# Kernel tuning notes

Hardware: AMD Instinct MI355X
Metric: run time of the kernel (lower is better)

Reference implementation:

```python
import jax, jax.numpy as jnp
import numpy as np

EMBED_DIM = 1024


def setup_inputs() -> dict:
    key = jax.random.key(0)
    ks = jax.random.split(key, 9)
    d = EMBED_DIM
    s = 1.0 / np.sqrt(d)
    x = jax.random.normal(ks[0], (4, 4096, d), dtype=jnp.float32)
    Wq = jax.random.normal(ks[1], (d, d), dtype=jnp.float32) * s
    bq = jax.random.normal(ks[2], (d,), dtype=jnp.float32) * 0.01
    Wk = jax.random.normal(ks[3], (d, d), dtype=jnp.float32) * s
    bk = jax.random.normal(ks[4], (d,), dtype=jnp.float32) * 0.01
    Wv = jax.random.normal(ks[5], (d, d), dtype=jnp.float32) * s
    bv = jax.random.normal(ks[6], (d,), dtype=jnp.float32) * 0.01
    Wo = jax.random.normal(ks[7], (d, d), dtype=jnp.float32) * s
    bo = jax.random.normal(ks[8], (d,), dtype=jnp.float32) * 0.01
    return {"x": x, "Wq": Wq, "bq": bq, "Wk": Wk, "bk": bk,
            "Wv": Wv, "bv": bv, "Wo": Wo, "bo": bo}


def reference(x, Wq, bq, Wk, bk, Wv, bv, Wo, bo):
    # x: [b, s, d]; single-head attention, scale = 1/sqrt(d)
    b, s, d = x.shape
    q = x @ Wq + bq
    k = x @ Wk + bk
    v = x @ Wv + bv
    scale = 1.0 / jnp.sqrt(jnp.asarray(d, x.dtype))
    scores = jnp.einsum('bqd,bkd->bqk', q, k) * scale  # [b, s, s]
    causal = jnp.tril(jnp.ones((s, s), dtype=bool))
    scores = jnp.where(causal, scores, jnp.asarray(-jnp.inf, scores.dtype))
    attn = jax.nn.softmax(scores, axis=-1)
    ctx = jnp.einsum('bqk,bkd->bqd', attn, v)
    return ctx @ Wo + bo
```

## Files before the change

### kernel.cpp

```cpp
#include <hip/hip_runtime.h>


typedef unsigned short u16;
typedef __attribute__((ext_vector_type(4))) unsigned short u16x4;
typedef __attribute__((ext_vector_type(8))) unsigned short u16x8;
typedef __attribute__((ext_vector_type(8))) __bf16 bf16x8;
typedef __attribute__((ext_vector_type(4))) float f32x4;

typedef const __attribute__((address_space(1))) void* as1cp;
typedef __attribute__((address_space(3))) void* as3p;

struct GemmPtrs {
  const u16* A[4];
  const u16* B[4];
  const float* bias[4];
  void* C[4];
};
struct TransPtrs {
  const void* in[4];
  u16* out[4];
};
struct SmPtrs {
  u16* P[4];
};

__device__ __forceinline__ u16 f2bf(float f) {
  union { float f; unsigned int i; } c; c.f = f;
  unsigned int r = c.i + 0x7fffu + ((c.i >> 16) & 1u);
  return (u16)(r >> 16);
}
__device__ __forceinline__ float bf2f(u16 u) {
  union { unsigned int i; float f; } c; c.i = ((unsigned int)u) << 16;
  return c.f;
}

__global__ __launch_bounds__(256) void cast_f32_bf16(const float* __restrict__ in,
                                                     u16* __restrict__ out, int n4) {
  int i = blockIdx.x * blockDim.x + threadIdx.x;
  if (i >= n4) return;
  float4 v = ((const float4*)in)[i];
  u16x4 u;
  u.x = f2bf(v.x); u.y = f2bf(v.y); u.z = f2bf(v.z); u.w = f2bf(v.w);
  ((u16x4*)out)[i] = u;
}

template <bool IN_F32>
__global__ __launch_bounds__(256) void transpose_to_bf16(TransPtrs tp, int R, int C) {
  __shared__ u16 t[32][34];
  int z = blockIdx.z;
  int tx = threadIdx.x, ty = threadIdx.y;
  int c0 = blockIdx.x * 32, r0 = blockIdx.y * 32;
#pragma unroll
  for (int dy = 0; dy < 4; ++dy) {
    int r = r0 + ty + dy * 8;
    int c = c0 + tx;
    u16 hv;
    if (IN_F32) hv = f2bf(((const float*)tp.in[z])[(size_t)r * C + c]);
    else        hv = ((const u16*)tp.in[z])[(size_t)r * C + c];
    t[ty + dy * 8][tx] = hv;
  }
  __syncthreads();
  u16* op = tp.out[z];
#pragma unroll
  for (int dy = 0; dy < 4; ++dy) {
    int a = ty + dy * 8;
    op[(size_t)(c0 + a) * R + r0 + tx] = t[tx][a];
  }
}

__global__ __launch_bounds__(256) void softmax_causal(SmPtrs sp) {
  int row = blockIdx.x;
  u16* P = sp.P[blockIdx.y];
  int tid = threadIdx.x;
  int lane = tid & 63, wv = tid >> 6;
  u16x8* prow = (u16x8*)(P + (size_t)row * 4096);
  int nch = (row >> 3) + 1;
  int fend = ((row >> 7) + 1) << 4;
  int c0 = tid, c1 = tid + 256;
  bool a0 = c0 < nch, a1 = c1 < nch;
  float vals[16];
  float lmax = -3.0e38f;
  if (a0) {
    u16x8 u = prow[c0];
#pragma unroll
    for (int e = 0; e < 8; ++e) {
      float f = (c0 * 8 + e <= row) ? bf2f(u[e]) : -3.0e38f;
      vals[e] = f; lmax = fmaxf(lmax, f);
    }
  } else {
#pragma unroll
    for (int e = 0; e < 8; ++e) vals[e] = -3.0e38f;
  }
  if (a1) {
    u16x8 u = prow[c1];
#pragma unroll
    for (int e = 0; e < 8; ++e) {
      float f = (c1 * 8 + e <= row) ? bf2f(u[e]) : -3.0e38f;
      vals[8 + e] = f; lmax = fmaxf(lmax, f);
    }
  } else {
#pragma unroll
    for (int e = 0; e < 8; ++e) vals[8 + e] = -3.0e38f;
  }
  __shared__ float red[8];
#pragma unroll
  for (int off = 32; off > 0; off >>= 1) lmax = fmaxf(lmax, __shfl_down(lmax, off, 64));
  if (lane == 0) red[wv] = lmax;
  __syncthreads();
  float m2 = fmaxf(fmaxf(red[0], red[1]), fmaxf(red[2], red[3]));
  float lsum = 0.f;
#pragma unroll
  for (int e = 0; e < 16; ++e) {
    float ev = __expf(vals[e] - m2);
    vals[e] = ev;
    lsum += ev;
  }
#pragma unroll
  for (int off = 32; off > 0; off >>= 1) lsum += __shfl_down(lsum, off, 64);
  if (lane == 0) red[4 + wv] = lsum;
  __syncthreads();
  float inv = 1.0f / (red[4] + red[5] + red[6] + red[7]);
  if (a0) {
    u16x8 u;
#pragma unroll
    for (int e = 0; e < 8; ++e) u[e] = f2bf(vals[e] * inv);
    prow[c0] = u;
  }
  if (a1) {
    u16x8 u;
#pragma unroll
    for (int e = 0; e < 8; ++e) u[e] = f2bf(vals[8 + e] * inv);
    prow[c1] = u;
  }
  u16x8 zz = (u16x8)(u16)0;
  for (int c = nch + tid; c < fend; c += 256) prow[c] = zz;
}

template <int MODE, bool OUT_BF16, bool HAS_BIAS, int MAXSLOT>
__global__ __launch_bounds__(256) void gemm_persist(GemmPtrs p, int K, int ldb, int N,
                                                    float cscale) {
  __shared__ __align__(16) u16 As[2][128 * 64];
  __shared__ __align__(16) u16 Bs[2][128 * 64];
  int b = blockIdx.x;
  int tid = threadIdx.x, lane = tid & 63, wv = tid >> 6;
  int wm = (wv >> 1) * 64, wn = (wv & 1) * 64;
  int lrow = lane & 15, lquad = lane >> 4;
  int srow = lane >> 3, scol = ((lane & 7) ^ srow) * 8;

  struct TP { const u16* A; const u16* B; int niter, tm, tn, z; };
  auto tileOf = [&](int s) {
    TP t;
    if (MODE == 0) {
      int tt = s * 512 + b; t.z = tt >> 10; int m = tt & 1023;
      t.tm = (m >> 3) << 7; t.tn = (m & 7) << 7; t.niter = K >> 6;
    } else if (MODE == 1) {
      int tt = (s < 4) ? s * 512 + b : 2048 + b;
      t.z = tt / 528; int L = tt - t.z * 528;
      int i = (int)((__fsqrt_rn(8.f * (float)L + 1.f) - 1.f) * 0.5f);
      while ((i + 1) * (i + 2) / 2 <= L) ++i;
      while (i * (i + 1) / 2 > L) --i;
      t.tm = i << 7; t.tn = (L - ((i * (i + 1)) >> 1)) << 7; t.niter = K >> 6;
    } else if (MODE == 2) {
      int g = b >> 5, w = b & 31; t.z = w >> 3;
      int i = (s == 0) ? 31 - g : g;
      t.tm = i << 7; t.tn = (w & 7) << 7; t.niter = (i + 1) * 2;
    } else {
      int tt = s * 512 + b; t.z = 0;
      t.tm = (tt >> 3) << 7; t.tn = (tt & 7) << 7; t.niter = K >> 6;
    }
    t.A = p.A[t.z] + (size_t)t.tm * K;
    t.B = p.B[t.z] + (size_t)t.tn * ldb;
    return t;
  };
  int nslot = (MODE == 1) ? (b < 64 ? 5 : 4) : MAXSLOT;
  int total = (MODE == 2) ? 66 : nslot * (K >> 6);

  auto stage = [&](const TP& t, int k0, int sb) {
#pragma unroll
    for (int tt = 0; tt < 4; ++tt) {
      int c = wv * 4 + tt;
      int ar = c * 8 + srow;
      const u16* ga = t.A + (size_t)ar * K + k0 + scol;
      __builtin_amdgcn_global_load_lds((as1cp)ga, (as3p)&As[sb][c * 512], 16, 0, 0);
      const u16* gb = t.B + (size_t)ar * ldb + k0 + scol;
      __builtin_amdgcn_global_load_lds((as1cp)gb, (as3p)&Bs[sb][c * 512], 16, 0, 0);
    }
  };

  f32x4 acc[4][4];
#pragma unroll
  for (int i = 0; i < 4; ++i)
#pragma unroll
    for (int j = 0; j < 4; ++j) acc[i][j] = (f32x4){0.f, 0.f, 0.f, 0.f};

  auto epi = [&](const TP& t) {
    const float* bias = HAS_BIAS ? p.bias[t.z] : nullptr;
#pragma unroll
    for (int mt = 0; mt < 4; ++mt) {
#pragma unroll
      for (int reg = 0; reg < 4; ++reg) {
        int r = t.tm + wm + mt * 16 + lquad * 4 + reg;
#pragma unroll
        for (int nt = 0; nt < 4; ++nt) {
          int cidx = t.tn + wn + nt * 16 + lrow;
          float vvv = acc[mt][nt][reg] * cscale;
          if (HAS_BIAS) vvv += bias[cidx];
          if (OUT_BF16) ((u16*)p.C[t.z])[(size_t)r * N + cidx] = f2bf(vvv);
          else          ((float*)p.C[t.z])[(size_t)r * N + cidx] = vvv;
        }
      }
    }
#pragma unroll
    for (int i = 0; i < 4; ++i)
#pragma unroll
      for (int j = 0; j < 4; ++j) acc[i][j] = (f32x4){0.f, 0.f, 0.f, 0.f};
  };

  TP st = tileOf(0);
  int stk = 0, sslot = 0;
  auto adv = [&]() {
    if (++stk == st.niter) {
      stk = 0;
      if (++sslot < nslot) st = tileOf(sslot);
    }
  };
  TP ct = st;
  int cit = 0, cslot = 0;

  stage(st, 0, 0);
  adv();
  for (int it = 0; it < total; ++it) {
    int cb = it & 1;
    if (it + 1 < total) {
      stage(st, stk << 6, cb ^ 1);
      adv();
      asm volatile("s_waitcnt vmcnt(8)" ::: "memory");
    } else {
      asm volatile("s_waitcnt vmcnt(0)" ::: "memory");
    }
    asm volatile("s_barrier" ::: "memory");
#pragma unroll
    for (int ks = 0; ks < 64; ks += 32) {
      bf16x8 af[4], bg[4];
#pragma unroll
      for (int mt = 0; mt < 4; ++mt) {
        int r = wm + mt * 16 + lrow;
        int jb = (ks >> 3) + lquad;
        af[mt] = *(const bf16x8*)&As[cb][r * 64 + ((jb ^ (r & 7)) << 3)];
      }
#pragma unroll
      for (int nt = 0; nt < 4; ++nt) {
        int r = wn + nt * 16 + lrow;
        int jb = (ks >> 3) + lquad;
        bg[nt] = *(const bf16x8*)&Bs[cb][r * 64 + ((jb ^ (r & 7)) << 3)];
      }
#pragma unroll
      for (int mt = 0; mt < 4; ++mt)
#pragma unroll
        for (int nt = 0; nt < 4; ++nt)
          acc[mt][nt] = __builtin_amdgcn_mfma_f32_16x16x32_bf16(af[mt], bg[nt], acc[mt][nt], 0, 0, 0);
    }
    asm volatile("s_barrier" ::: "memory");
    if (++cit == ct.niter) {
      epi(ct);
      cit = 0;
      if (++cslot < nslot) ct = tileOf(cslot);
    }
  }
}

extern "C" void kernel_launch(void* const* d_in, const int* in_sizes, int n_in,
                              void* d_out, int out_size, void* d_ws, size_t ws_size,
                              hipStream_t stream) {
  const float* x  = (const float*)d_in[0];
  const float* Wq = (const float*)d_in[1];
  const float* bq = (const float*)d_in[2];
  const float* Wk = (const float*)d_in[3];
  const float* bk = (const float*)d_in[4];
  const float* Wv = (const float*)d_in[5];
  const float* bv = (const float*)d_in[6];
  const float* Wo = (const float*)d_in[7];
  const float* bo = (const float*)d_in[8];

  const int S = 4096, D = 1024;
  const size_t XE = (size_t)4 * S * D;
  const size_t BSE = (size_t)S * D;

  char* ws = (char*)d_ws;
  u16* xb  = (u16*)(ws + 0);
  u16* q   = (u16*)(ws + 33554432);
  u16* k   = (u16*)(ws + 67108864);
  u16* v   = (u16*)(ws + 100663296);
  u16* ctx = (u16*)(ws + 134217728);
  u16* wqT = (u16*)(ws + 167772160);
  u16* wkT = wqT + 1048576;
  u16* wvT = wkT + 1048576;
  u16* woT = wvT + 1048576;
  u16* attn2 = (u16*)(ws + 176160768);
  u16* attn0 = (u16*)d_out;
  u16* attn1 = attn0 + (size_t)S * S;
  u16* attn3 = v;
  u16* vT = xb;
  u16* attn[4] = {attn0, attn1, attn2, attn3};

  cast_f32_bf16<<<(int)(XE / 4 / 256), 256, 0, stream>>>(x, xb, (int)(XE / 4));
  {
    TransPtrs tp = {{Wq, Wk, Wv, Wo}, {wqT, wkT, wvT, woT}};
    transpose_to_bf16<true><<<dim3(32, 32, 4), dim3(32, 8), 0, stream>>>(tp, D, D);
  }
  {
    GemmPtrs gp = {{xb, xb, xb, xb}, {wqT, wkT, wvT, wqT},
                   {bq, bk, bv, bq}, {q, k, v, q}};
    gemm_persist<0, true, true, 6><<<512, 256, 0, stream>>>(gp, D, D, D, 1.0f);
  }
  {
    TransPtrs tp = {{v, v + BSE, v + 2 * BSE, v + 3 * BSE},
                    {vT, vT + BSE, vT + 2 * BSE, vT + 3 * BSE}};
    transpose_to_bf16<false><<<dim3(D / 32, S / 32, 4), dim3(32, 8), 0, stream>>>(tp, S, D);
  }
  {
    GemmPtrs gp = {{q, q + BSE, q + 2 * BSE, q + 3 * BSE},
                   {k, k + BSE, k + 2 * BSE, k + 3 * BSE},
                   {nullptr, nullptr, nullptr, nullptr},
                   {attn[0], attn[1], attn[2], attn[3]}};
    gemm_persist<1, true, false, 5><<<512, 256, 0, stream>>>(gp, D, D, S, 0.03125f);
  }
  {
    SmPtrs sp = {{attn[0], attn[1], attn[2], attn[3]}};
    softmax_causal<<<dim3(S, 4), 256, 0, stream>>>(sp);
  }
  {
    GemmPtrs gp = {{attn[0], attn[1], attn[2], attn[3]},
                   {vT, vT + BSE, vT + 2 * BSE, vT + 3 * BSE},
                   {nullptr, nullptr, nullptr, nullptr},
                   {ctx, ctx + BSE, ctx + 2 * BSE, ctx + 3 * BSE}};
    gemm_persist<2, true, false, 2><<<512, 256, 0, stream>>>(gp, S, S, D, 1.0f);
  }
  {
    GemmPtrs gp = {{ctx, ctx, ctx, ctx}, {woT, woT, woT, woT},
                   {bo, bo, bo, bo}, {d_out, d_out, d_out, d_out}};
    gemm_persist<3, false, true, 2><<<512, 256, 0, stream>>>(gp, D, D, D, 1.0f);
  }
}
```

Before: 614.8 us.

## Remap persistent GEMM tiles per XCD and make K/ldb compile-time

Block-to-tile mapping in all four GEMM modes now uses b&7 (the XCD index under round-robin dispatch) so that blocks sharing an A row-tile or B column-tile land on the same XCD. The aim is better L2 reuse on the chiplet. K and ldb also become template parameters, so address arithmetic is constant-folded. The risk is load imbalance or worse reuse if the XCD assignment assumption does not hold.

```diff
diff --git a/kernel.cpp b/kernel.cpp
--- a/kernel.cpp
+++ b/kernel.cpp
@@ -136,12 +136,12 @@
   for (int c = nch + tid; c < fend; c += 256) prow[c] = zz;
 }
 
-template <int MODE, bool OUT_BF16, bool HAS_BIAS, int MAXSLOT>
-__global__ __launch_bounds__(256) void gemm_persist(GemmPtrs p, int K, int ldb, int N,
-                                                    float cscale) {
+template <int MODE, bool OUT_BF16, bool HAS_BIAS, int MAXSLOT, int KDIM, int LDB>
+__global__ __launch_bounds__(256) void gemm_persist(GemmPtrs p, int N, float cscale) {
   __shared__ __align__(16) u16 As[2][128 * 64];
   __shared__ __align__(16) u16 Bs[2][128 * 64];
   int b = blockIdx.x;
+  int x = b & 7, q = b >> 3;
   int tid = threadIdx.x, lane = tid & 63, wv = tid >> 6;
   int wm = (wv >> 1) * 64, wn = (wv & 1) * 64;
   int lrow = lane & 15, lquad = lane >> 4;
@@ -151,38 +151,40 @@
   auto tileOf = [&](int s) {
     TP t;
     if (MODE == 0) {
-      int tt = s * 512 + b; t.z = tt >> 10; int m = tt & 1023;
-      t.tm = (m >> 3) << 7; t.tn = (m & 7) << 7; t.niter = K >> 6;
+      int c = x + 8 * (s * 8 + (q >> 3));
+      t.z = c >> 7;
+      t.tm = (c & 127) << 7; t.tn = (q & 7) << 7; t.niter = KDIM >> 6;
     } else if (MODE == 1) {
-      int tt = (s < 4) ? s * 512 + b : 2048 + b;
+      int c = x + 8 * (s * 8 + (q >> 3));
+      int tt = c * 8 + (q & 7);
       t.z = tt / 528; int L = tt - t.z * 528;
       int i = (int)((__fsqrt_rn(8.f * (float)L + 1.f) - 1.f) * 0.5f);
       while ((i + 1) * (i + 2) / 2 <= L) ++i;
       while (i * (i + 1) / 2 > L) --i;
-      t.tm = i << 7; t.tn = (L - ((i * (i + 1)) >> 1)) << 7; t.niter = K >> 6;
+      t.tm = i << 7; t.tn = (L - ((i * (i + 1)) >> 1)) << 7; t.niter = KDIM >> 6;
     } else if (MODE == 2) {
-      int g = b >> 5, w = b & 31; t.z = w >> 3;
-      int i = (s == 0) ? 31 - g : g;
-      t.tm = i << 7; t.tn = (w & 7) << 7; t.niter = (i + 1) * 2;
+      int w = q & 15, h = w >> 3;
+      int i = (s == 0) ? (h ? 15 - x : x) : (h ? 16 + x : 31 - x);
+      t.z = q >> 4; t.tm = i << 7; t.tn = (w & 7) << 7; t.niter = (i + 1) * 2;
     } else {
-      int tt = s * 512 + b; t.z = 0;
-      t.tm = (tt >> 3) << 7; t.tn = (tt & 7) << 7; t.niter = K >> 6;
-    }
-    t.A = p.A[t.z] + (size_t)t.tm * K;
-    t.B = p.B[t.z] + (size_t)t.tn * ldb;
+      int c = x + 8 * (s * 8 + (q >> 3));
+      t.z = 0; t.tm = c << 7; t.tn = (q & 7) << 7; t.niter = KDIM >> 6;
+    }
+    t.A = p.A[t.z] + (size_t)t.tm * KDIM;
+    t.B = p.B[t.z] + (size_t)t.tn * LDB;
     return t;
   };
-  int nslot = (MODE == 1) ? (b < 64 ? 5 : 4) : MAXSLOT;
-  int total = (MODE == 2) ? 66 : nslot * (K >> 6);
+  int nslot = (MODE == 1) ? ((q >> 3) == 0 ? 5 : 4) : MAXSLOT;
+  int total = (MODE == 2) ? 66 : nslot * (KDIM >> 6);
 
   auto stage = [&](const TP& t, int k0, int sb) {
 #pragma unroll
     for (int tt = 0; tt < 4; ++tt) {
       int c = wv * 4 + tt;
       int ar = c * 8 + srow;
-      const u16* ga = t.A + (size_t)ar * K + k0 + scol;
+      const u16* ga = t.A + (size_t)ar * KDIM + k0 + scol;
       __builtin_amdgcn_global_load_lds((as1cp)ga, (as3p)&As[sb][c * 512], 16, 0, 0);
-      const u16* gb = t.B + (size_t)ar * ldb + k0 + scol;
+      const u16* gb = t.B + (size_t)ar * LDB + k0 + scol;
       __builtin_amdgcn_global_load_lds((as1cp)gb, (as3p)&Bs[sb][c * 512], 16, 0, 0);
     }
   };
@@ -311,7 +313,7 @@
   {
     GemmPtrs gp = {{xb, xb, xb, xb}, {wqT, wkT, wvT, wqT},
                    {bq, bk, bv, bq}, {q, k, v, q}};
-    gemm_persist<0, true, true, 6><<<512, 256, 0, stream>>>(gp, D, D, D, 1.0f);
+    gemm_persist<0, true, true, 6, 1024, 1024><<<512, 256, 0, stream>>>(gp, D, 1.0f);
   }
   {
     TransPtrs tp = {{v, v + BSE, v + 2 * BSE, v + 3 * BSE},
@@ -323,7 +325,7 @@
                    {k, k + BSE, k + 2 * BSE, k + 3 * BSE},
                    {nullptr, nullptr, nullptr, nullptr},
                    {attn[0], attn[1], attn[2], attn[3]}};
-    gemm_persist<1, true, false, 5><<<512, 256, 0, stream>>>(gp, D, D, S, 0.03125f);
+    gemm_persist<1, true, false, 5, 1024, 1024><<<512, 256, 0, stream>>>(gp, S, 0.03125f);
   }
   {
     SmPtrs sp = {{attn[0], attn[1], attn[2], attn[3]}};
@@ -334,11 +336,11 @@
                    {vT, vT + BSE, vT + 2 * BSE, vT + 3 * BSE},
                    {nullptr, nullptr, nullptr, nullptr},
                    {ctx, ctx + BSE, ctx + 2 * BSE, ctx + 3 * BSE}};
-    gemm_persist<2, true, false, 2><<<512, 256, 0, stream>>>(gp, S, S, D, 1.0f);
+    gemm_persist<2, true, false, 2, 4096, 4096><<<512, 256, 0, stream>>>(gp, D, 1.0f);
   }
   {
     GemmPtrs gp = {{ctx, ctx, ctx, ctx}, {woT, woT, woT, woT},
                    {bo, bo, bo, bo}, {d_out, d_out, d_out, d_out}};
-    gemm_persist<3, false, true, 2><<<512, 256, 0, stream>>>(gp, D, D, D, 1.0f);
-  }
-}
+    gemm_persist<3, false, true, 2, 1024, 1024><<<512, 256, 0, stream>>>(gp, D, 1.0f);
+  }
+}
```

After: 572.9 us. -6.8%, faster.
